# Performance work log

Hardware: AMD Instinct MI355X
Metric: run time of the kernel (lower is better)

The kernel has to match this reference:

```python
import jax, jax.numpy as jnp
import numpy as np

N, D, H, E = 8192, 1024, 4096, 8


def setup_inputs() -> dict:
    key = jax.random.key(0)
    ks = jax.random.split(key, 5)
    s_in = 1.0 / np.sqrt(D)
    s_h = 1.0 / np.sqrt(H)
    return {
        "x": jax.random.normal(ks[0], (N, D), dtype=jnp.float32),
        "Wg": jax.random.normal(ks[1], (D, E), dtype=jnp.float32) * s_in,
        "bg": jnp.zeros((E,), dtype=jnp.float32),
        "W1": jax.random.normal(ks[2], (E, D, H), dtype=jnp.float32) * s_in,
        "b1": jnp.zeros((E, H), dtype=jnp.float32),
        "W2": jax.random.normal(ks[3], (E, H, D), dtype=jnp.float32) * s_h,
        "b2": jnp.zeros((E, D), dtype=jnp.float32),
    }


def reference(x, Wg, bg, W1, b1, W2, b2):
    # gate: softmax linear router -> weights [N, E]
    weights = jax.nn.softmax(x @ Wg + bg, axis=-1)
    # all experts, batched GEMMs: h [N, E, H]
    h = jax.nn.relu(jnp.einsum("nd,edh->neh", x, W1) + b1)  # Dropout is identity at inference
    outputs = jnp.einsum("neh,ehd->ned", h, W2) + b2         # [N, E, D]
    # weighted combine over experts
    return jnp.einsum("ne,ned->nd", weights, outputs)
```

## Files before the change

### kernel.cpp

```cpp
#include <hip/hip_runtime.h>
#include <hip/hip_bf16.h>

#define DDIM 1024
#define HDIM 4096
#define NEXP 8
#define NROW 8192
#define KPAIR 8192

typedef __attribute__((ext_vector_type(8))) short s16x8;
typedef __attribute__((ext_vector_type(4))) float f32x4;

using bf16 = __hip_bfloat16;

__device__ __forceinline__ void gload16(const bf16* g, bf16* lds) {
    __builtin_amdgcn_global_load_lds(
        (const __attribute__((address_space(1))) unsigned int*)g,
        (__attribute__((address_space(3))) unsigned int*)lds,
        16, 0, 0);
}

template <int N>
__device__ __forceinline__ void wait_vmcnt() {
    if constexpr (N == 6)      asm volatile("s_waitcnt vmcnt(6)" ::: "memory");
    else if constexpr (N == 3) asm volatile("s_waitcnt vmcnt(3)" ::: "memory");
    else                       asm volatile("s_waitcnt vmcnt(0)" ::: "memory");
}

__global__ void cvtgate_kernel(const float* __restrict__ x, const float* __restrict__ Wg,
                               const float* __restrict__ bg, const float* __restrict__ b2,
                               bf16* __restrict__ xb, float* __restrict__ wts,
                               float* __restrict__ out) {
    int wave = threadIdx.x >> 6, lane = threadIdx.x & 63;
    int n = blockIdx.x * 4 + wave;
    const float* xr = x + (size_t)n * DDIM;
    bf16* xbr = xb + (size_t)n * DDIM;
    float acc[NEXP] = {0.f, 0.f, 0.f, 0.f, 0.f, 0.f, 0.f, 0.f};
#pragma unroll
    for (int j = 0; j < 4; ++j) {
        int d0 = j * 256 + lane * 4;
        float4 v = *(const float4*)&xr[d0];
        union { bf16 b[4]; uint2 u; } pk;
        pk.b[0] = __float2bfloat16(v.x);
        pk.b[1] = __float2bfloat16(v.y);
        pk.b[2] = __float2bfloat16(v.z);
        pk.b[3] = __float2bfloat16(v.w);
        *(uint2*)&xbr[d0] = pk.u;
        const float* w0 = Wg + (size_t)d0 * NEXP;
#pragma unroll
        for (int e = 0; e < NEXP; ++e)
            acc[e] += v.x * w0[e] + v.y * w0[NEXP + e] + v.z * w0[2 * NEXP + e] +
                      v.w * w0[3 * NEXP + e];
    }
#pragma unroll
    for (int off = 32; off > 0; off >>= 1) {
#pragma unroll
        for (int e = 0; e < NEXP; ++e) acc[e] += __shfl_xor(acc[e], off, 64);
    }
    float mx = -1e30f;
#pragma unroll
    for (int e = 0; e < NEXP; ++e) { acc[e] += bg[e]; mx = fmaxf(mx, acc[e]); }
    float s = 0.f;
#pragma unroll
    for (int e = 0; e < NEXP; ++e) { acc[e] = __expf(acc[e] - mx); s += acc[e]; }
    float inv = 1.0f / s;
#pragma unroll
    for (int e = 0; e < NEXP; ++e) acc[e] *= inv;
    if (lane == 0) {
#pragma unroll
        for (int e = 0; e < NEXP; ++e) wts[(size_t)n * NEXP + e] = acc[e];
    }
    float* outr = out + (size_t)n * DDIM;
#pragma unroll
    for (int j = 0; j < 4; ++j) {
        int d0 = j * 256 + lane * 4;
        float4 sum = {0.f, 0.f, 0.f, 0.f};
#pragma unroll
        for (int e = 0; e < NEXP; ++e) {
            float4 bv = *(const float4*)&b2[(size_t)e * DDIM + d0];
            sum.x += acc[e] * bv.x;
            sum.y += acc[e] * bv.y;
            sum.z += acc[e] * bv.z;
            sum.w += acc[e] * bv.w;
        }
        *(float4*)&outr[d0] = sum;
    }
}

__global__ void transpose_pair_kernel(const float* __restrict__ W1s, bf16* __restrict__ W1d,
                                      const float* __restrict__ W2s, bf16* __restrict__ W2d) {
    __shared__ float t[128][65];
    const int z = blockIdx.z;
    const float* src; bf16* dst; int C, ldo, bx, by;
    if (z < 2) {
        src = W1s + (size_t)z * DDIM * HDIM;
        dst = W1d + (size_t)z * HDIM * DDIM;
        C = HDIM; ldo = DDIM;
        bx = blockIdx.x & 31; by = blockIdx.x >> 5;
    } else {
        src = W2s + (size_t)(z - 2) * HDIM * DDIM;
        dst = W2d + (size_t)(z - 2) * HDIM;
        C = DDIM; ldo = KPAIR;
        bx = blockIdx.x & 7; by = blockIdx.x >> 3;
    }
    const int r0 = by * 64, c0 = bx * 128;
    const int tid = threadIdx.x;
    const int lrow = tid >> 5, lc4 = tid & 31;
#pragma unroll
    for (int i = 0; i < 8; ++i) {
        int rr = i * 8 + lrow;
        float4 v = *(const float4*)&src[(size_t)(r0 + rr) * C + c0 + lc4 * 4];
        t[lc4 * 4 + 0][rr] = v.x;
        t[lc4 * 4 + 1][rr] = v.y;
        t[lc4 * 4 + 2][rr] = v.z;
        t[lc4 * 4 + 3][rr] = v.w;
    }
    __syncthreads();
    const int oc = tid >> 3, oj = tid & 7;
#pragma unroll
    for (int i = 0; i < 4; ++i) {
        int c = oc + i * 32;
        union { bf16 b[8]; s16x8 v; } p;
#pragma unroll
        for (int q = 0; q < 8; ++q) p.b[q] = __float2bfloat16(t[c][oj * 8 + q]);
        *(s16x8*)&dst[(size_t)(c0 + c) * ldo + r0 + oj * 8] = p.v;
    }
}

__global__ __launch_bounds__(512, 1) void gemm1(
    const bf16* __restrict__ A, const bf16* __restrict__ BTp, bf16* __restrict__ Hsb,
    const float* __restrict__ b1p, const float* __restrict__ wts,
    int lda, int ldb, int ldc, int NT, int tilesM, int tilesN, int XGN, int e0) {
    constexpr int WROWS = 128;
    constexpr int HALFA = 256 * 32;
    constexpr int HALFB = 256 * 32;
    constexpr int ATOT = 2 * HALFA;
    constexpr int BUFE = ATOT + 2 * HALFB;
    __shared__ __align__(16) bf16 smem[2 * BUFE];

    const int tid = threadIdx.x;
    const int wave = tid >> 6, lane = tid & 63;
    const int wm = wave >> 2, wn = wave & 3;
    const int r = lane & 15, kg = lane >> 4;

    const int eh = blockIdx.x >> 9;
    const int bx = blockIdx.x & 511;
    const bf16* BT = BTp + (size_t)eh * HDIM * DDIM;
    bf16* Cout = Hsb + (size_t)eh * HDIM;
    const float* bias = b1p + (size_t)eh * HDIM;
    const int expert = e0 + eh;

    const int xcd = bx & 7, slot = bx >> 3;
    const int XGM = 8 / XGN;
    const int rm = tilesM / XGM, rn = tilesN / XGN;
    const int g = slot >> 5, u = slot & 31;
    const int gpr = rn >> 3;
    const int gm = (g / gpr) * 4 + (u >> 3);
    const int gn = (g % gpr) * 8 + (u & 7);
    const int tm = (xcd / XGN) * rm + gm;
    const int tn = (xcd % XGN) * rn + gn;

    const bf16* gA = A + (size_t)tm * 256 * lda;
    const bf16* gB = BT + (size_t)tn * 256 * ldb;

    f32x4 acc[8][4];
#pragma unroll
    for (int m = 0; m < 8; ++m)
#pragma unroll
        for (int n = 0; n < 4; ++n) acc[m][n] = (f32x4){0.f, 0.f, 0.f, 0.f};

    auto stageA = [&](int t, int ks) {
        bf16* dst = smem + (t & 1) * BUFE + ks * HALFA;
#pragma unroll
        for (int j = 0; j < 2; ++j) {
            int c = j * 512 + tid;
            int R = c >> 2, kc = (c & 3) ^ ((R >> 1) & 3);
            gload16(gA + (size_t)R * lda + t * 64 + ks * 32 + kc * 8,
                    dst + (j * 512 + wave * 64) * 8);
        }
    };
    auto stageB = [&](int t, int ks) {
        bf16* dst = smem + (t & 1) * BUFE + ATOT + ks * HALFB;
#pragma unroll
        for (int j = 0; j < 2; ++j) {
            int c = j * 512 + tid;
            int R = c >> 2, kc = (c & 3) ^ ((R >> 1) & 3);
            gload16(gB + (size_t)R * ldb + t * 64 + ks * 32 + kc * 8,
                    dst + (j * 512 + wave * 64) * 8);
        }
    };

    s16x8 a0[4], bb[4];
    auto ldA = [&](int buf, int ks, int mh) {
#pragma unroll
        for (int m = 0; m < 4; ++m) {
            int R = wm * WROWS + mh * 64 + m * 16 + r;
            a0[m] = *(const s16x8*)&smem[buf * BUFE + ks * HALFA + R * 32 +
                                         ((kg ^ ((R >> 1) & 3)) * 8)];
        }
    };
    auto ldB = [&](int buf, int ks) {
#pragma unroll
        for (int n = 0; n < 4; ++n) {
            int R = wn * 64 + n * 16 + r;
            bb[n] = *(const s16x8*)&smem[buf * BUFE + ATOT + ks * HALFB + R * 32 +
                                         ((kg ^ ((R >> 1) & 3)) * 8)];
        }
    };

    auto preMFMA = [&]() {
        __builtin_amdgcn_s_barrier();
        asm volatile("s_waitcnt lgkmcnt(0)" ::: "memory");
        __builtin_amdgcn_sched_barrier(0);
        __builtin_amdgcn_s_setprio(1);
    };
    auto postMFMA = [&](bool vm) {
        __builtin_amdgcn_s_setprio(0);
        if (vm) wait_vmcnt<6>();
        __builtin_amdgcn_s_barrier();
    };
    auto mfmaLo = [&]() {
#pragma unroll
        for (int m = 0; m < 4; ++m)
#pragma unroll
            for (int n = 0; n < 4; ++n)
                acc[m][n] = __builtin_amdgcn_mfma_f32_16x16x32_bf16(a0[m], bb[n], acc[m][n], 0, 0, 0);
    };
    auto mfmaHi = [&]() {
#pragma unroll
        for (int m = 0; m < 4; ++m)
#pragma unroll
            for (int n = 0; n < 4; ++n)
                acc[4 + m][n] = __builtin_amdgcn_mfma_f32_16x16x32_bf16(a0[m], bb[n], acc[4 + m][n], 0, 0, 0);
    };

    stageB(0, 0); stageA(0, 0); stageB(0, 1); stageA(0, 1);
    stageB(1, 0); stageA(1, 0); stageB(1, 1);
    wait_vmcnt<6>();
    __builtin_amdgcn_s_barrier();

    const int NI = NT / 2;
    for (int i = 0; i < NI; ++i) {
        const int t0 = 2 * i, t1 = t0 + 1;
        const bool g2 = (t0 + 2 < NT), g3 = (t1 + 2 < NT);
        ldB(0, 0); ldA(0, 0, 0); stageA(t1, 1);
        preMFMA(); mfmaLo(); postMFMA(false);
        ldA(0, 0, 1); if (g2) stageB(t0 + 2, 0);
        preMFMA(); mfmaHi(); postMFMA(false);
        ldB(0, 1); ldA(0, 1, 0); if (g2) stageA(t0 + 2, 0);
        preMFMA(); mfmaLo(); postMFMA(false);
        ldA(0, 1, 1); if (g2) stageB(t0 + 2, 1);
        preMFMA(); mfmaHi(); postMFMA(true);
        ldB(1, 0); ldA(1, 0, 0); if (g2) stageA(t0 + 2, 1);
        preMFMA(); mfmaLo(); postMFMA(false);
        ldA(1, 0, 1); if (g3) stageB(t1 + 2, 0);
        preMFMA(); mfmaHi(); postMFMA(false);
        ldB(1, 1); ldA(1, 1, 0); if (g3) stageA(t1 + 2, 0);
        preMFMA(); mfmaLo(); postMFMA(false);
        ldA(1, 1, 1); if (g3) stageB(t1 + 2, 1);
        preMFMA(); mfmaHi(); postMFMA(true);
    }

    bf16* hs = smem;
    const int col0 = tn * 256 + wn * 64;
#pragma unroll
    for (int n = 0; n < 4; ++n) {
        float bv = bias[col0 + n * 16 + r];
        int cl = wn * 64 + n * 16 + r;
#pragma unroll
        for (int mf = 0; mf < 8; ++mf) {
#pragma unroll
            for (int j = 0; j < 4; ++j) {
                int rl = wm * WROWS + (mf >> 2) * 64 + (mf & 3) * 16 + kg * 4 + j;
                float wv = wts[((size_t)tm * 256 + rl) * NEXP + expert];
                float v = acc[mf][n][j] + bv;
                v = v > 0.f ? v : 0.f;
                hs[rl * 256 + (cl ^ ((rl & 7) << 3))] = __float2bfloat16(wv * v);
            }
        }
    }
    __builtin_amdgcn_s_barrier();
    asm volatile("s_waitcnt lgkmcnt(0)" ::: "memory");
    const size_t rbase = (size_t)tm * 256;
    const int cbase = tn * 256;
#pragma unroll
    for (int i2 = 0; i2 < 16; ++i2) {
        int rl = wave * 32 + i2 * 2 + (lane >> 5);
        int c8 = (lane & 31) * 8;
        s16x8 v = *(const s16x8*)&hs[rl * 256 + (c8 ^ ((rl & 7) << 3))];
        *(s16x8*)&Cout[(rbase + rl) * (size_t)ldc + cbase + c8] = v;
    }
}

__global__ __launch_bounds__(256, 2) void gemm2p(
    const bf16* __restrict__ A, const bf16* __restrict__ BT, float* __restrict__ O,
    int lda, int ldb, int ldc, int NT, int tilesM, int tilesN, int XGN) {
    constexpr int HALFA = 128 * 32;
    constexpr int HALFB = 128 * 32;
    constexpr int ATOT = 2 * HALFA;
    constexpr int BUFE = ATOT + 2 * HALFB;
    constexpr int RSTR = 68;
    __shared__ __align__(16) bf16 smem[2 * BUFE];

    const int tid = threadIdx.x;
    const int wave = tid >> 6, lane = tid & 63;
    const int ksw = wave & 1, wn = wave >> 1;
    const int r = lane & 15, kg = lane >> 4;

    const int xcd = blockIdx.x & 7, slot = blockIdx.x >> 3;
    const int XGM = 8 / XGN;
    const int rm = tilesM / XGM, rn = tilesN / XGN;
    const int g = slot >> 5, u = slot & 31;
    const int gpr = rn >> 3;
    const int gm = (g / gpr) * 4 + (u >> 3);
    const int gn = (g % gpr) * 8 + (u & 7);
    const int tm = (xcd / XGN) * rm + gm;
    const int tn = (xcd % XGN) * rn + gn;

    const bf16* gA = A + (size_t)tm * 128 * lda;
    const bf16* gB = BT + (size_t)tn * 128 * ldb;

    f32x4 acc[8][4];
#pragma unroll
    for (int m = 0; m < 8; ++m)
#pragma unroll
        for (int n = 0; n < 4; ++n) acc[m][n] = (f32x4){0.f, 0.f, 0.f, 0.f};

    auto stageA_rh = [&](int t, int rh) {
        bf16* base = smem + (t & 1) * BUFE;
#pragma unroll
        for (int j = 0; j < 2; ++j) {
            int c = j * 256 + tid;
            int Rl = (c >> 2) & 63;
            int R = rh * 64 + Rl;
            int kc = (c & 3) ^ ((R >> 1) & 3);
            gload16(gA + (size_t)R * lda + t * 64 + j * 32 + kc * 8,
                    base + j * HALFA + rh * 2048 + ((c & 255) - lane) * 8 + lane * 8);
        }
    };
    auto stageB = [&](int t) {
        bf16* base = smem + (t & 1) * BUFE + ATOT;
#pragma unroll
        for (int j = 0; j < 4; ++j) {
            int c = j * 256 + tid;
            int ks = c >> 9;
            int R = (c >> 2) & 127;
            int kc = (c & 3) ^ ((R >> 1) & 3);
            gload16(gB + (size_t)R * ldb + t * 64 + ks * 32 + kc * 8,
                    base + ks * HALFB + ((c & 511) - lane) * 8 + lane * 8);
        }
    };

    s16x8 afr[4], bfr[4];
    auto ldA = [&](int b, int mh) {
#pragma unroll
        for (int m = 0; m < 4; ++m) {
            int R = mh * 64 + m * 16 + r;
            afr[m] = *(const s16x8*)&smem[b * BUFE + ksw * HALFA + R * 32 +
                                          ((kg ^ ((R >> 1) & 3)) * 8)];
        }
    };
    auto ldB = [&](int b) {
#pragma unroll
        for (int n = 0; n < 4; ++n) {
            int R = wn * 64 + n * 16 + r;
            bfr[n] = *(const s16x8*)&smem[b * BUFE + ATOT + ksw * HALFB + R * 32 +
                                          ((kg ^ ((R >> 1) & 3)) * 8)];
        }
    };

    auto preMFMA = [&]() {
        __builtin_amdgcn_s_barrier();
        asm volatile("s_waitcnt lgkmcnt(0)" ::: "memory");
        __builtin_amdgcn_sched_barrier(0);
        __builtin_amdgcn_s_setprio(1);
    };

    stageA_rh(0, 0); stageA_rh(0, 1); stageB(0);
    stageA_rh(1, 1); stageB(1);
    wait_vmcnt<6>();
    __builtin_amdgcn_s_barrier();

    for (int t = 0; t < NT; ++t) {
        const int b = t & 1;
        ldB(b); ldA(b, 1);
        if (t + 1 < NT) stageA_rh(t + 1, 0);
        preMFMA();
#pragma unroll
        for (int m = 0; m < 4; ++m)
#pragma unroll
            for (int n = 0; n < 4; ++n)
                acc[4 + m][n] = __builtin_amdgcn_mfma_f32_16x16x32_bf16(afr[m], bfr[n], acc[4 + m][n], 0, 0, 0);
        __builtin_amdgcn_s_setprio(0);
        __builtin_amdgcn_s_barrier();
        ldA(b, 0);
        if (t + 2 < NT) { stageA_rh(t + 2, 1); stageB(t + 2); }
        preMFMA();
#pragma unroll
        for (int m = 0; m < 4; ++m)
#pragma unroll
            for (int n = 0; n < 4; ++n)
                acc[m][n] = __builtin_amdgcn_mfma_f32_16x16x32_bf16(afr[m], bfr[n], acc[m][n], 0, 0, 0);
        __builtin_amdgcn_s_setprio(0);
        if (t + 1 < NT) {
            if (t + 2 < NT) wait_vmcnt<6>();
            else            wait_vmcnt<0>();
            __builtin_amdgcn_s_barrier();
        }
    }

    __syncthreads();
    float* red = (float*)smem;
    const int zone = wn * (64 * RSTR);
    const int col0 = tn * 128 + wn * 64;
    const size_t row0 = (size_t)tm * 128;
    if (ksw == 1) {
#pragma unroll
        for (int mq = 0; mq < 4; ++mq)
#pragma unroll
            for (int n = 0; n < 4; ++n) {
                int rl = mq * 16 + kg * 4;
                int cl = n * 16 + r;
#pragma unroll
                for (int j = 0; j < 4; ++j)
                    red[zone + (rl + j) * RSTR + cl] = acc[mq][n][j];
            }
    }
    __syncthreads();
    if (ksw == 0) {
#pragma unroll
        for (int mq = 0; mq < 4; ++mq)
#pragma unroll
            for (int j = 0; j < 4; ++j) {
                int rl = mq * 16 + kg * 4 + j;
                size_t rr = row0 + rl;
#pragma unroll
                for (int n = 0; n < 4; ++n) {
                    int cl = n * 16 + r;
                    O[rr * (size_t)ldc + col0 + cl] += acc[mq][n][j] + red[zone + rl * RSTR + cl];
                }
            }
    }
    __syncthreads();
    if (ksw == 0) {
#pragma unroll
        for (int mq = 0; mq < 4; ++mq)
#pragma unroll
            for (int n = 0; n < 4; ++n) {
                int rl = mq * 16 + kg * 4;
                int cl = n * 16 + r;
#pragma unroll
                for (int j = 0; j < 4; ++j)
                    red[zone + (rl + j) * RSTR + cl] = acc[4 + mq][n][j];
            }
    }
    __syncthreads();
    if (ksw == 1) {
#pragma unroll
        for (int mq = 0; mq < 4; ++mq)
#pragma unroll
            for (int j = 0; j < 4; ++j) {
                int rl = mq * 16 + kg * 4 + j;
                size_t rr = row0 + 64 + rl;
#pragma unroll
                for (int n = 0; n < 4; ++n) {
                    int cl = n * 16 + r;
                    O[rr * (size_t)ldc + col0 + cl] += acc[4 + mq][n][j] + red[zone + rl * RSTR + cl];
                }
            }
    }
}

extern "C" void kernel_launch(void* const* d_in, const int* in_sizes, int n_in,
                              void* d_out, int out_size, void* d_ws, size_t ws_size,
                              hipStream_t stream) {
    const float* x  = (const float*)d_in[0];
    const float* Wg = (const float*)d_in[1];
    const float* bg = (const float*)d_in[2];
    const float* W1 = (const float*)d_in[3];
    const float* b1 = (const float*)d_in[4];
    const float* W2 = (const float*)d_in[5];
    const float* b2 = (const float*)d_in[6];
    float* out = (float*)d_out;

    char* ws = (char*)d_ws;
    bf16* xb   = (bf16*)(ws);
    bf16* W1P  = (bf16*)(ws + (16ull << 20));
    bf16* W2P  = (bf16*)(ws + (32ull << 20));
    bf16* Hs   = (bf16*)(ws + (48ull << 20));
    float* wts = (float*)(ws + (176ull << 20));

    cvtgate_kernel<<<NROW / 4, 256, 0, stream>>>(x, Wg, bg, b2, xb, wts, out);

    for (int p = 0; p < 4; ++p) {
        transpose_pair_kernel<<<dim3(512, 1, 4), 256, 0, stream>>>(
            W1 + (size_t)2 * p * DDIM * HDIM, W1P,
            W2 + (size_t)2 * p * HDIM * DDIM, W2P);
        gemm1<<<1024, 512, 0, stream>>>(
            xb, W1P, Hs, b1 + (size_t)2 * p * HDIM, wts,
            DDIM, DDIM, KPAIR, DDIM / 64, 32, 16, 2, 2 * p);
        gemm2p<<<512, 256, 0, stream>>>(
            Hs, W2P, out, KPAIR, KPAIR, DDIM, KPAIR / 64, 64, 8, 1);
    }
}
```

Measured before the change: 1.229 ms.

## Restructure GEMM main loop to one barrier per K-tile with separate A fragments

Replaces the two-phase inner loop, with its staggered half-tile prefetch two steps ahead and two barriers per tile, by a simpler schedule. Each tile now loads all B and both A halves into separate registers (a0, a1), prefetches the entire next tile, waits on partial LDS counts, and uses a single barrier. The intent is fewer barriers and waits per iteration and overlap of the second half's LDS reads with the first half's MFMAs. In exchange it uses more registers, shortens prefetch depth to one tile, and waits on all outstanding global loads each iteration, which may expose memory latency.

```diff
diff --git a/kernel.cpp b/kernel.cpp
--- a/kernel.cpp
+++ b/kernel.cpp
@@ -350,13 +350,21 @@
         }
     };
 
-    s16x8 afr[4], bfr[4];
-    auto ldA = [&](int b, int mh) {
+    s16x8 a0[4], a1[4], bfr[4];
+    auto ldA0 = [&](int b) {
 #pragma unroll
         for (int m = 0; m < 4; ++m) {
-            int R = mh * 64 + m * 16 + r;
-            afr[m] = *(const s16x8*)&smem[b * BUFE + ksw * HALFA + R * 32 +
-                                          ((kg ^ ((R >> 1) & 3)) * 8)];
+            int R = m * 16 + r;
+            a0[m] = *(const s16x8*)&smem[b * BUFE + ksw * HALFA + R * 32 +
+                                         ((kg ^ ((R >> 1) & 3)) * 8)];
+        }
+    };
+    auto ldA1 = [&](int b) {
+#pragma unroll
+        for (int m = 0; m < 4; ++m) {
+            int R = 64 + m * 16 + r;
+            a1[m] = *(const s16x8*)&smem[b * BUFE + ksw * HALFA + R * 32 +
+                                         ((kg ^ ((R >> 1) & 3)) * 8)];
         }
     };
     auto ldB = [&](int b) {
@@ -368,42 +376,34 @@
         }
     };
 
-    auto preMFMA = [&]() {
-        __builtin_amdgcn_s_barrier();
+    stageA_rh(0, 0); stageA_rh(0, 1); stageB(0);
+    wait_vmcnt<0>();
+    __builtin_amdgcn_s_barrier();
+
+    for (int t = 0; t < NT; ++t) {
+        const int b = t & 1;
+        ldB(b); ldA1(b); ldA0(b);
+        if (t + 1 < NT) { stageA_rh(t + 1, 0); stageA_rh(t + 1, 1); stageB(t + 1); }
+        asm volatile("s_waitcnt lgkmcnt(4)" ::: "memory");
+        __builtin_amdgcn_sched_barrier(0);
+        __builtin_amdgcn_s_setprio(1);
+#pragma unroll
+        for (int m = 0; m < 4; ++m)
+#pragma unroll
+            for (int n = 0; n < 4; ++n)
+                acc[4 + m][n] = __builtin_amdgcn_mfma_f32_16x16x32_bf16(a1[m], bfr[n], acc[4 + m][n], 0, 0, 0);
+        __builtin_amdgcn_s_setprio(0);
         asm volatile("s_waitcnt lgkmcnt(0)" ::: "memory");
         __builtin_amdgcn_sched_barrier(0);
         __builtin_amdgcn_s_setprio(1);
-    };
-
-    stageA_rh(0, 0); stageA_rh(0, 1); stageB(0);
-    stageA_rh(1, 1); stageB(1);
-    wait_vmcnt<6>();
-    __builtin_amdgcn_s_barrier();
-
-    for (int t = 0; t < NT; ++t) {
-        const int b = t & 1;
-        ldB(b); ldA(b, 1);
-        if (t + 1 < NT) stageA_rh(t + 1, 0);
-        preMFMA();
 #pragma unroll
         for (int m = 0; m < 4; ++m)
 #pragma unroll
             for (int n = 0; n < 4; ++n)
-                acc[4 + m][n] = __builtin_amdgcn_mfma_f32_16x16x32_bf16(afr[m], bfr[n], acc[4 + m][n], 0, 0, 0);
-        __builtin_amdgcn_s_setprio(0);
-        __builtin_amdgcn_s_barrier();
-        ldA(b, 0);
-        if (t + 2 < NT) { stageA_rh(t + 2, 1); stageB(t + 2); }
-        preMFMA();
-#pragma unroll
-        for (int m = 0; m < 4; ++m)
-#pragma unroll
-            for (int n = 0; n < 4; ++n)
-                acc[m][n] = __builtin_amdgcn_mfma_f32_16x16x32_bf16(afr[m], bfr[n], acc[m][n], 0, 0, 0);
+                acc[m][n] = __builtin_amdgcn_mfma_f32_16x16x32_bf16(a0[m], bfr[n], acc[m][n], 0, 0, 0);
         __builtin_amdgcn_s_setprio(0);
         if (t + 1 < NT) {
-            if (t + 2 < NT) wait_vmcnt<6>();
-            else            wait_vmcnt<0>();
+            wait_vmcnt<0>();
             __builtin_amdgcn_s_barrier();
         }
     }
```

New measurement: 1.221 ms. No clear change (-0.6%).
